# Performance work log

Measured on AMD Instinct MI355X. Metric: run time of the kernel, lower is better.

The kernel has to match this reference:

```python
import jax, jax.numpy as jnp
import numpy as np

N_NODES = 100000
N_EDGES = 3200000
N_FEAT = 128
DIM = 48
N_CLASS = 18
BN_EPS = 1e-5


def setup_inputs() -> dict:
    key = jax.random.key(0)
    ks = jax.random.split(key, 20)
    x = jax.random.normal(ks[0], (N_NODES, N_FEAT), dtype=jnp.float32)
    edge_index = jax.random.randint(ks[1], (2, N_EDGES), 0, N_NODES, dtype=jnp.int64)

    def lin(k, fan_in, fan_out):
        s = 1.0 / np.sqrt(fan_in)
        kw, kb = jax.random.split(k)
        W = jax.random.uniform(kw, (fan_in, fan_out), jnp.float32, -s, s)
        b = jax.random.uniform(kb, (fan_out,), jnp.float32, -s, s)
        return W, b

    c1_W1, c1_b1 = lin(ks[2], N_FEAT, DIM)
    c1_W2, c1_b2 = lin(ks[3], DIM, DIM)
    c2_W1, c2_b1 = lin(ks[4], DIM, DIM)
    c2_W2, c2_b2 = lin(ks[5], DIM, DIM)
    fc1_W, fc1_b = lin(ks[6], DIM, DIM)
    fc2_W, fc2_b = lin(ks[7], DIM, N_CLASS)

    def bn(k):
        k1, k2, k3, k4 = jax.random.split(k, 4)
        gamma = 1.0 + 0.1 * jax.random.normal(k1, (DIM,), jnp.float32)
        beta = 0.1 * jax.random.normal(k2, (DIM,), jnp.float32)
        mean = 0.1 * jax.random.normal(k3, (DIM,), jnp.float32)
        var = jax.random.uniform(k4, (DIM,), jnp.float32, 0.5, 1.5)
        return gamma, beta, mean, var

    bn1_g, bn1_b, bn1_m, bn1_v = bn(ks[8])
    bn2_g, bn2_b, bn2_m, bn2_v = bn(ks[9])

    return {
        "x": x, "edge_index": edge_index,
        "c1_W1": c1_W1, "c1_b1": c1_b1, "c1_W2": c1_W2, "c1_b2": c1_b2,
        "c2_W1": c2_W1, "c2_b1": c2_b1, "c2_W2": c2_W2, "c2_b2": c2_b2,
        "bn1_g": bn1_g, "bn1_b": bn1_b, "bn1_m": bn1_m, "bn1_v": bn1_v,
        "bn2_g": bn2_g, "bn2_b": bn2_b, "bn2_m": bn2_m, "bn2_v": bn2_v,
        "fc1_W": fc1_W, "fc1_b": fc1_b, "fc2_W": fc2_W, "fc2_b": fc2_b,
    }


def _gine_conv(x, src, dst, W1, b1, W2, b2, eps=0.0):
    # PyG GINEConv (edge_attr absent): message = ReLU(x_j), sum-aggregate to dst,
    # then nn((1+eps)*x + aggr) where nn = Linear-ReLU-Linear.
    msg = jax.nn.relu(x[src])                                  # [E, F]
    aggr = jax.ops.segment_sum(msg, dst, num_segments=x.shape[0])  # [N, F]
    h = (1.0 + eps) * x + aggr
    return jax.nn.relu(h @ W1 + b1) @ W2 + b2


def _bn_eval(x, gamma, beta, mean, var):
    return (x - mean) * (gamma * jax.lax.rsqrt(var + BN_EPS)) + beta


def reference(x, edge_index,
              c1_W1, c1_b1, c1_W2, c1_b2,
              c2_W1, c2_b1, c2_W2, c2_b2,
              bn1_g, bn1_b, bn1_m, bn1_v,
              bn2_g, bn2_b, bn2_m, bn2_v,
              fc1_W, fc1_b, fc2_W, fc2_b):
    src, dst = edge_index[0], edge_index[1]
    h = jax.nn.relu(_gine_conv(x, src, dst, c1_W1, c1_b1, c1_W2, c1_b2))
    h = _bn_eval(h, bn1_g, bn1_b, bn1_m, bn1_v)
    h = jax.nn.relu(_gine_conv(h, src, dst, c2_W1, c2_b1, c2_W2, c2_b2))
    h = _bn_eval(h, bn2_g, bn2_b, bn2_m, bn2_v)
    h = jax.nn.relu(h @ fc1_W + fc1_b)
    # dropout is identity in eval mode
    return h @ fc2_W + fc2_b
```

## Files before the change

### kernel.cpp

```cpp
#include <hip/hip_runtime.h>
#include <hip/hip_fp16.h>

#define N_NODES 100000
#define N_EDGES 3200000
#define N_FEAT  128
#define DIM     48
#define N_CLASS 18
#define BN_EPS  1e-5f

#define PADW 136
#define PADC 72
#define MROW 64

#define BSH    7
#define BROWS  128
#define NBUCK  ((N_NODES + BROWS - 1) / BROWS)
#define BCAP   4608
#define EPB    4096
#define NBLK_E ((N_EDGES + EPB - 1) / EPB)

typedef __attribute__((ext_vector_type(8))) _Float16 f16x8;
typedef __attribute__((ext_vector_type(4))) float f32x4;



__global__ __launch_bounds__(256) void k_bin(const int* __restrict__ ei,
                                             int* __restrict__ bcursor,
                                             unsigned int* __restrict__ pairs) {
    __shared__ int h[NBUCK];
    __shared__ int pos[NBUCK];
    const int t = threadIdx.x;
    const int bs = blockIdx.x * EPB;
    const int ce = min(EPB, N_EDGES - bs);

    int sv[16], dv[16];
    #pragma unroll
    for (int i = 0; i < 16; i++) {
        int e = t + i * 256;
        if (e < ce) { sv[i] = ei[bs + e]; dv[i] = ei[N_EDGES + bs + e]; }
        else { sv[i] = 0; dv[i] = -1; }
    }
    for (int i = t; i < NBUCK; i += 256) h[i] = 0;
    __syncthreads();
    #pragma unroll
    for (int i = 0; i < 16; i++)
        if (dv[i] >= 0) atomicAdd(&h[dv[i] >> BSH], 1);
    __syncthreads();

    for (int b = t; b < NBUCK; b += 256) {
        int cnt = h[b];
        if (cnt > 0) {
            int g = atomicAdd(&bcursor[b], cnt);
            h[b] = b * BCAP + g;
        }
        pos[b] = 0;
    }
    __syncthreads();

    #pragma unroll
    for (int i = 0; i < 16; i++) {
        if (dv[i] >= 0) {
            int b = dv[i] >> BSH;
            int p = atomicAdd(&pos[b], 1);
            pairs[h[b] + p] = ((unsigned int)sv[i] << 7) | (unsigned int)(dv[i] & (BROWS - 1));
        }
    }
}


__global__ __launch_bounds__(256) void k_sort(const unsigned int* __restrict__ pairs,
                                              const int* __restrict__ bcursor,
                                              int* __restrict__ row_beg,
                                              int* __restrict__ row_end,
                                              int* __restrict__ sorted_src) {
    __shared__ int histw[4 * BROWS];
    __shared__ int woff[4 * BROWS];
    __shared__ int tot[BROWS];
    __shared__ int scn[BROWS];
    __shared__ int beg[BROWS];
    const int t = threadIdx.x;
    const int wid = t >> 6;
    const int b = blockIdx.x;
    const int nbase = b << BSH;
    const int start_w = b * BCAP;
    const int cnt = bcursor[b];

    for (int i = t; i < 4 * BROWS; i += 256) histw[i] = 0;
    __syncthreads();
    for (int e = start_w + t; e < start_w + cnt; e += 256)
        atomicAdd(&histw[wid * BROWS + (pairs[e] & (BROWS - 1))], 1);
    __syncthreads();

    if (t < BROWS) {
        int run = 0;
        #pragma unroll
        for (int w = 0; w < 4; w++) {
            woff[w * BROWS + t] = run;
            run += histw[w * BROWS + t];
        }
        tot[t] = run;
        scn[t] = run;
    }
    __syncthreads();
    for (int off = 1; off < BROWS; off <<= 1) {
        int v = 0;
        if (t < BROWS && t >= off) v = scn[t - off];
        __syncthreads();
        if (t < BROWS) scn[t] += v;
        __syncthreads();
    }
    if (t < BROWS) {
        int rb = start_w + scn[t] - tot[t];
        beg[t] = rb;
        int n = nbase + t;
        if (n < N_NODES) {
            row_beg[n] = rb;
            row_end[n] = rb + tot[t];
        }
    }
    __syncthreads();
    if (t < BROWS) {
        #pragma unroll
        for (int w = 0; w < 4; w++)
            histw[w * BROWS + t] = beg[t] + woff[w * BROWS + t];
    }
    __syncthreads();
    for (int e = start_w + t; e < start_w + cnt; e += 256) {
        unsigned int p = pairs[e];
        int node = p & (BROWS - 1);
        int idx = atomicAdd(&histw[wid * BROWS + node], 1);
        sorted_src[idx] = (int)(p >> 7);
    }
}


__global__ __launch_bounds__(256) void k_g1(const float* __restrict__ x,
                                            const float* __restrict__ W1,
                                            __half* __restrict__ t1,
                                            __half* __restrict__ t2) {
    __shared__ _Float16 sX[64 * PADW];
    __shared__ _Float16 sW[DIM * PADW];
    const int t = threadIdx.x;
    const int base = blockIdx.x * 64;
    const int wid = t >> 6, lane = t & 63;

    for (int idx = t; idx < DIM * (N_FEAT / 2); idx += 256) {
        int c = idx >> 6;
        int kk = (idx & 63) * 2;
        *(__half2*)&sW[c * PADW + kk] =
            __floats2half2_rn(W1[kk * DIM + c], W1[(kk + 1) * DIM + c]);
    }
    #pragma unroll
    for (int i = 0; i < 8; i++) {
        int idx = t + i * 256;
        int row = idx >> 5, kq = idx & 31;
        float4 v = make_float4(0.f, 0.f, 0.f, 0.f);
        if (base + row < N_NODES) v = ((const float4*)x)[(base + row) * 32 + kq];
        *(__half2*)&sX[row * PADW + kq * 4]     = __floats2half2_rn(v.x, v.y);
        *(__half2*)&sX[row * PADW + kq * 4 + 2] = __floats2half2_rn(v.z, v.w);
    }
    __syncthreads();

    const int r16 = wid * 16;
    const int lrow = lane & 15;
    const int lk = (lane >> 4) * 8;

    f32x4 acc1[3], acc2[3];
    #pragma unroll
    for (int c = 0; c < 3; c++) {
        acc1[c] = (f32x4){0.f, 0.f, 0.f, 0.f};
        acc2[c] = (f32x4){0.f, 0.f, 0.f, 0.f};
    }

    #pragma unroll
    for (int ks = 0; ks < 4; ks++) {
        f16x8 a = *(const f16x8*)&sX[(r16 + lrow) * PADW + ks * 32 + lk];
        f16x8 ra;
        #pragma unroll
        for (int j = 0; j < 8; j++)
            ra[j] = a[j] > (_Float16)0 ? a[j] : (_Float16)0;
        #pragma unroll
        for (int c = 0; c < 3; c++) {
            f16x8 b = *(const f16x8*)&sW[(c * 16 + lrow) * PADW + ks * 32 + lk];
            acc1[c] = __builtin_amdgcn_mfma_f32_16x16x32_f16(a,  b, acc1[c], 0, 0, 0);
            acc2[c] = __builtin_amdgcn_mfma_f32_16x16x32_f16(ra, b, acc2[c], 0, 0, 0);
        }
    }

    const int orow = r16 + (lane >> 4) * 4;
    const int ocol = lane & 15;
    #pragma unroll
    for (int q = 0; q < 4; q++) {
        int gr = base + orow + q;
        if (gr < N_NODES) {
            #pragma unroll
            for (int c = 0; c < 3; c++) {
                t1[gr * DIM + c * 16 + ocol] = __float2half(acc1[c][q]);
                t2[gr * MROW + c * 16 + ocol] = __float2half(acc2[c][q]);
            }
        }
    }
}


__device__ inline float2 h2tof2(unsigned int u) {
    __half2 h = *reinterpret_cast<__half2*>(&u);
    return __half22float2(h);
}

__global__ __launch_bounds__(256) void k_aggr(const uint2* tl8,
                                              const uint2* __restrict__ tmsg8,
                                              const int* __restrict__ row_beg,
                                              const int* __restrict__ row_end,
                                              const int* __restrict__ ssrc,
                                              const float* __restrict__ bias,
                                              uint2* out8) {
    const int t = threadIdx.x;
    const int wid = t >> 6, lane = t & 63;
    const int sub = lane / 12;
    const int fl  = lane - sub * 12;
    int n = blockIdx.x * 20 + wid * 5 + sub;
    const bool act = (sub < 5) && (n < N_NODES);
    int start = 0, end = 0;
    if (act) { start = row_beg[n]; end = row_end[n]; }

    float ax = 0.f, ay = 0.f, az = 0.f, aw = 0.f;
    int e = start;
    for (; e + 8 <= end; e += 8) {
        int s0 = ssrc[e], s1 = ssrc[e + 1], s2 = ssrc[e + 2], s3 = ssrc[e + 3];
        int s4 = ssrc[e + 4], s5 = ssrc[e + 5], s6 = ssrc[e + 6], s7 = ssrc[e + 7];
        uint2 v0 = tmsg8[s0 * 16 + fl];
        uint2 v1 = tmsg8[s1 * 16 + fl];
        uint2 v2 = tmsg8[s2 * 16 + fl];
        uint2 v3 = tmsg8[s3 * 16 + fl];
        uint2 v4 = tmsg8[s4 * 16 + fl];
        uint2 v5 = tmsg8[s5 * 16 + fl];
        uint2 v6 = tmsg8[s6 * 16 + fl];
        uint2 v7 = tmsg8[s7 * 16 + fl];
        float2 f;
        f = h2tof2(v0.x); ax += f.x; ay += f.y;  f = h2tof2(v0.y); az += f.x; aw += f.y;
        f = h2tof2(v1.x); ax += f.x; ay += f.y;  f = h2tof2(v1.y); az += f.x; aw += f.y;
        f = h2tof2(v2.x); ax += f.x; ay += f.y;  f = h2tof2(v2.y); az += f.x; aw += f.y;
        f = h2tof2(v3.x); ax += f.x; ay += f.y;  f = h2tof2(v3.y); az += f.x; aw += f.y;
        f = h2tof2(v4.x); ax += f.x; ay += f.y;  f = h2tof2(v4.y); az += f.x; aw += f.y;
        f = h2tof2(v5.x); ax += f.x; ay += f.y;  f = h2tof2(v5.y); az += f.x; aw += f.y;
        f = h2tof2(v6.x); ax += f.x; ay += f.y;  f = h2tof2(v6.y); az += f.x; aw += f.y;
        f = h2tof2(v7.x); ax += f.x; ay += f.y;  f = h2tof2(v7.y); az += f.x; aw += f.y;
    }
    for (; e < end; e++) {
        int s = ssrc[e];
        uint2 v = tmsg8[s * 16 + fl];
        float2 f;
        f = h2tof2(v.x); ax += f.x; ay += f.y;
        f = h2tof2(v.y); az += f.x; aw += f.y;
    }
    if (act) {
        uint2 tv = tl8[n * 12 + fl];
        float2 b0 = h2tof2(tv.x), b1 = h2tof2(tv.y);
        float4 bi = ((const float4*)bias)[fl];
        float rx = fmaxf(b0.x + ax + bi.x, 0.f);
        float ry = fmaxf(b0.y + ay + bi.y, 0.f);
        float rz = fmaxf(b1.x + az + bi.z, 0.f);
        float rw = fmaxf(b1.y + aw + bi.w, 0.f);
        uint2 o;
        __half2 h0 = __floats2half2_rn(rx, ry);
        __half2 h1 = __floats2half2_rn(rz, rw);
        o.x = *reinterpret_cast<unsigned int*>(&h0);
        o.y = *reinterpret_cast<unsigned int*>(&h1);
        out8[n * 12 + fl] = o;
    }
}


__global__ __launch_bounds__(256) void k_chain1(const __half* u,
                                                const float* __restrict__ W2,
                                                const float* __restrict__ b2,
                                                const float* __restrict__ bng,
                                                const float* __restrict__ bnb,
                                                const float* __restrict__ bnm,
                                                const float* __restrict__ bnv,
                                                const float* __restrict__ W1n,
                                                __half* t3,
                                                __half* __restrict__ t4) {
    __shared__ _Float16 sU[64 * PADC];
    __shared__ _Float16 sG[64 * PADC];
    __shared__ _Float16 sW2t[DIM * PADC];
    __shared__ _Float16 sW1t[DIM * PADC];
    __shared__ float sb2[DIM], ssc[DIM], ssh[DIM];
    const int t = threadIdx.x;
    const int base = blockIdx.x * 64;
    const int wid = t >> 6, lane = t & 63;

    if (t < DIM) {
        sb2[t] = b2[t];
        float sc = bng[t] * rsqrtf(bnv[t] + BN_EPS);
        ssc[t] = sc;
        ssh[t] = bnb[t] - bnm[t] * sc;
    }
    for (int idx = t; idx < DIM * 24; idx += 256) {
        int c = idx / 24, kk = (idx - c * 24) * 2;
        sW2t[c * PADC + kk]     = (_Float16)W2[kk * DIM + c];
        sW2t[c * PADC + kk + 1] = (_Float16)W2[(kk + 1) * DIM + c];
        sW1t[c * PADC + kk]     = (_Float16)W1n[kk * DIM + c];
        sW1t[c * PADC + kk + 1] = (_Float16)W1n[(kk + 1) * DIM + c];
    }
    for (int idx = t; idx < DIM * 16; idx += 256) {
        int c = idx >> 4, j = idx & 15;
        sW2t[c * PADC + 48 + j] = (_Float16)0;
        sW1t[c * PADC + 48 + j] = (_Float16)0;
    }
    for (int idx = t; idx < 64 * 16; idx += 256) {
        int r = idx >> 4, j = idx & 15;
        sU[r * PADC + 48 + j] = (_Float16)0;
        sG[r * PADC + 48 + j] = (_Float16)0;
    }
    for (int idx = t; idx < 64 * 12; idx += 256) {
        int row = idx / 12, kk = idx - row * 12;
        uint2 v = make_uint2(0u, 0u);
        if (base + row < N_NODES) v = ((const uint2*)u)[(base + row) * 12 + kk];
        *(uint2*)&sU[row * PADC + kk * 4] = v;
    }
    __syncthreads();

    const int r16 = wid * 16;
    const int lrow = lane & 15;
    const int lk = (lane >> 4) * 8;
    const int orow = r16 + (lane >> 4) * 4;
    const int ocol = lane & 15;

    f32x4 av[3];
    #pragma unroll
    for (int c = 0; c < 3; c++) av[c] = (f32x4){0.f, 0.f, 0.f, 0.f};
    #pragma unroll
    for (int ks = 0; ks < 2; ks++) {
        f16x8 a = *(const f16x8*)&sU[(r16 + lrow) * PADC + ks * 32 + lk];
        #pragma unroll
        for (int c = 0; c < 3; c++) {
            f16x8 b = *(const f16x8*)&sW2t[(c * 16 + lrow) * PADC + ks * 32 + lk];
            av[c] = __builtin_amdgcn_mfma_f32_16x16x32_f16(a, b, av[c], 0, 0, 0);
        }
    }
    #pragma unroll
    for (int c = 0; c < 3; c++) {
        int col = c * 16 + ocol;
        float bb = sb2[col], sc = ssc[col], sh = ssh[col];
        #pragma unroll
        for (int q = 0; q < 4; q++) {
            float rl = fmaxf(av[c][q] + bb, 0.f);
            sG[(orow + q) * PADC + col] = (_Float16)(rl * sc + sh);
        }
    }
    __syncthreads();

    f32x4 a3[3], a4[3];
    #pragma unroll
    for (int c = 0; c < 3; c++) {
        a3[c] = (f32x4){0.f, 0.f, 0.f, 0.f};
        a4[c] = (f32x4){0.f, 0.f, 0.f, 0.f};
    }
    #pragma unroll
    for (int ks = 0; ks < 2; ks++) {
        f16x8 a = *(const f16x8*)&sG[(r16 + lrow) * PADC + ks * 32 + lk];
        f16x8 ra;
        #pragma unroll
        for (int j = 0; j < 8; j++)
            ra[j] = a[j] > (_Float16)0 ? a[j] : (_Float16)0;
        #pragma unroll
        for (int c = 0; c < 3; c++) {
            f16x8 b = *(const f16x8*)&sW1t[(c * 16 + lrow) * PADC + ks * 32 + lk];
            a3[c] = __builtin_amdgcn_mfma_f32_16x16x32_f16(a,  b, a3[c], 0, 0, 0);
            a4[c] = __builtin_amdgcn_mfma_f32_16x16x32_f16(ra, b, a4[c], 0, 0, 0);
        }
    }
    #pragma unroll
    for (int q = 0; q < 4; q++) {
        int gr = base + orow + q;
        if (gr < N_NODES) {
            #pragma unroll
            for (int c = 0; c < 3; c++) {
                t3[gr * DIM + c * 16 + ocol] = __float2half(a3[c][q]);
                t4[gr * MROW + c * 16 + ocol] = __float2half(a4[c][q]);
            }
        }
    }
}


__global__ __launch_bounds__(256) void k_chain2(const __half* __restrict__ u2,
                                                const float* __restrict__ W2,
                                                const float* __restrict__ b2,
                                                const float* __restrict__ bng,
                                                const float* __restrict__ bnb,
                                                const float* __restrict__ bnm,
                                                const float* __restrict__ bnv,
                                                const float* __restrict__ fc1W,
                                                const float* __restrict__ fc1b,
                                                const float* __restrict__ fc2W,
                                                const float* __restrict__ fc2b,
                                                float* __restrict__ out) {
    __shared__ _Float16 sA[64 * PADC];
    __shared__ _Float16 sG[64 * PADC];
    __shared__ _Float16 sWa[DIM * PADC];
    __shared__ _Float16 sWb[DIM * PADC];
    __shared__ _Float16 sWc[32 * PADC];
    __shared__ float sb2[DIM], ssc[DIM], ssh[DIM], sfb1[DIM], sfb2[N_CLASS];
    const int t = threadIdx.x;
    const int base = blockIdx.x * 64;
    const int wid = t >> 6, lane = t & 63;

    if (t < DIM) {
        sb2[t] = b2[t];
        float sc = bng[t] * rsqrtf(bnv[t] + BN_EPS);
        ssc[t] = sc;
        ssh[t] = bnb[t] - bnm[t] * sc;
        sfb1[t] = fc1b[t];
    }
    if (t >= 64 && t < 64 + N_CLASS) sfb2[t - 64] = fc2b[t - 64];

    for (int idx = t; idx < DIM * 24; idx += 256) {
        int c = idx / 24, kk = (idx - c * 24) * 2;
        sWa[c * PADC + kk]     = (_Float16)W2[kk * DIM + c];
        sWa[c * PADC + kk + 1] = (_Float16)W2[(kk + 1) * DIM + c];
        sWb[c * PADC + kk]     = (_Float16)fc1W[kk * DIM + c];
        sWb[c * PADC + kk + 1] = (_Float16)fc1W[(kk + 1) * DIM + c];
    }
    for (int idx = t; idx < DIM * 16; idx += 256) {
        int c = idx >> 4, j = idx & 15;
        sWa[c * PADC + 48 + j] = (_Float16)0;
        sWb[c * PADC + 48 + j] = (_Float16)0;
    }
    for (int idx = t; idx < N_CLASS * DIM; idx += 256) {
        int c = idx / DIM, k = idx - c * DIM;
        sWc[c * PADC + k] = (_Float16)fc2W[k * N_CLASS + c];
    }
    for (int idx = t; idx < 32 * 16; idx += 256) {
        int c = idx >> 4, j = idx & 15;
        sWc[c * PADC + 48 + j] = (_Float16)0;
    }
    for (int idx = t; idx < 14 * 48; idx += 256) {
        int c = 18 + idx / 48, k = idx - (idx / 48) * 48;
        sWc[c * PADC + k] = (_Float16)0;
    }
    for (int idx = t; idx < 64 * 16; idx += 256) {
        int r = idx >> 4, j = idx & 15;
        sA[r * PADC + 48 + j] = (_Float16)0;
        sG[r * PADC + 48 + j] = (_Float16)0;
    }
    for (int idx = t; idx < 64 * 12; idx += 256) {
        int row = idx / 12, kk = idx - row * 12;
        uint2 v = make_uint2(0u, 0u);
        if (base + row < N_NODES) v = ((const uint2*)u2)[(base + row) * 12 + kk];
        *(uint2*)&sA[row * PADC + kk * 4] = v;
    }
    __syncthreads();

    const int r16 = wid * 16;
    const int lrow = lane & 15;
    const int lk = (lane >> 4) * 8;
    const int orow = r16 + (lane >> 4) * 4;
    const int ocol = lane & 15;

    {
        f32x4 av[3];
        #pragma unroll
        for (int c = 0; c < 3; c++) av[c] = (f32x4){0.f, 0.f, 0.f, 0.f};
        #pragma unroll
        for (int ks = 0; ks < 2; ks++) {
            f16x8 a = *(const f16x8*)&sA[(r16 + lrow) * PADC + ks * 32 + lk];
            #pragma unroll
            for (int c = 0; c < 3; c++) {
                f16x8 b = *(const f16x8*)&sWa[(c * 16 + lrow) * PADC + ks * 32 + lk];
                av[c] = __builtin_amdgcn_mfma_f32_16x16x32_f16(a, b, av[c], 0, 0, 0);
            }
        }
        #pragma unroll
        for (int c = 0; c < 3; c++) {
            int col = c * 16 + ocol;
            float bb = sb2[col], sc = ssc[col], sh = ssh[col];
            #pragma unroll
            for (int q = 0; q < 4; q++) {
                float rl = fmaxf(av[c][q] + bb, 0.f);
                sG[(orow + q) * PADC + col] = (_Float16)(rl * sc + sh);
            }
        }
    }
    __syncthreads();

    {
        f32x4 az[3];
        #pragma unroll
        for (int c = 0; c < 3; c++) az[c] = (f32x4){0.f, 0.f, 0.f, 0.f};
        #pragma unroll
        for (int ks = 0; ks < 2; ks++) {
            f16x8 a = *(const f16x8*)&sG[(r16 + lrow) * PADC + ks * 32 + lk];
            #pragma unroll
            for (int c = 0; c < 3; c++) {
                f16x8 b = *(const f16x8*)&sWb[(c * 16 + lrow) * PADC + ks * 32 + lk];
                az[c] = __builtin_amdgcn_mfma_f32_16x16x32_f16(a, b, az[c], 0, 0, 0);
            }
        }
        __syncthreads();
        #pragma unroll
        for (int c = 0; c < 3; c++) {
            int col = c * 16 + ocol;
            float bb = sfb1[col];
            #pragma unroll
            for (int q = 0; q < 4; q++)
                sA[(orow + q) * PADC + col] = (_Float16)fmaxf(az[c][q] + bb, 0.f);
        }
    }
    __syncthreads();

    {
        f32x4 ao[2];
        #pragma unroll
        for (int c = 0; c < 2; c++) ao[c] = (f32x4){0.f, 0.f, 0.f, 0.f};
        #pragma unroll
        for (int ks = 0; ks < 2; ks++) {
            f16x8 a = *(const f16x8*)&sA[(r16 + lrow) * PADC + ks * 32 + lk];
            #pragma unroll
            for (int c = 0; c < 2; c++) {
                f16x8 b = *(const f16x8*)&sWc[(c * 16 + lrow) * PADC + ks * 32 + lk];
                ao[c] = __builtin_amdgcn_mfma_f32_16x16x32_f16(a, b, ao[c], 0, 0, 0);
            }
        }
        #pragma unroll
        for (int q = 0; q < 4; q++) {
            int gr = base + orow + q;
            if (gr < N_NODES) {
                #pragma unroll
                for (int c = 0; c < 2; c++) {
                    int col = c * 16 + ocol;
                    if (col < N_CLASS)
                        out[gr * N_CLASS + col] = ao[c][q] + sfb2[col];
                }
            }
        }
    }
}


extern "C" void kernel_launch(void* const* d_in, const int* in_sizes, int n_in,
                              void* d_out, int out_size, void* d_ws, size_t ws_size,
                              hipStream_t stream) {
    const float* x     = (const float*)d_in[0];
    const int*   ei    = (const int*)d_in[1];
    const float* c1_W1 = (const float*)d_in[2];
    const float* c1_b1 = (const float*)d_in[3];
    const float* c1_W2 = (const float*)d_in[4];
    const float* c1_b2 = (const float*)d_in[5];
    const float* c2_W1 = (const float*)d_in[6];
    const float* c2_b1 = (const float*)d_in[7];
    const float* c2_W2 = (const float*)d_in[8];
    const float* c2_b2 = (const float*)d_in[9];
    const float* bn1_g = (const float*)d_in[10];
    const float* bn1_b = (const float*)d_in[11];
    const float* bn1_m = (const float*)d_in[12];
    const float* bn1_v = (const float*)d_in[13];
    const float* bn2_g = (const float*)d_in[14];
    const float* bn2_b = (const float*)d_in[15];
    const float* bn2_m = (const float*)d_in[16];
    const float* bn2_v = (const float*)d_in[17];
    const float* fc1_W = (const float*)d_in[18];
    const float* fc1_b = (const float*)d_in[19];
    const float* fc2_W = (const float*)d_in[20];
    const float* fc2_b = (const float*)d_in[21];
    float* out = (float*)d_out;

    char* ws = (char*)d_ws;
    size_t o = 0;
    auto take = [&](size_t bytes) {
        void* p = ws + o;
        o = (o + bytes + 255) & ~(size_t)255;
        return p;
    };
    unsigned int* pairs = (unsigned int*)take((size_t)NBUCK * BCAP * 4);
    int*  sorted_src    = (int*)take((size_t)NBUCK * BCAP * 4);
    int*  row_beg       = (int*)take((size_t)N_NODES * 4);
    int*  row_end       = (int*)take((size_t)N_NODES * 4);
    int*  bcursor       = (int*)take((size_t)NBUCK * 4);
    __half* t1h         = (__half*)take((size_t)N_NODES * DIM * 2);
    __half* t2h         = (__half*)take((size_t)N_NODES * MROW * 2);
    (void)ws_size; (void)in_sizes; (void)n_in; (void)out_size;

    const int NB64 = (N_NODES + 63) / 64;
    const int NB20 = (N_NODES + 19) / 20;

    hipMemsetAsync(bcursor, 0, (size_t)NBUCK * 4, stream);
    k_bin<<<NBLK_E, 256, 0, stream>>>(ei, bcursor, pairs);
    k_sort<<<NBUCK, 256, 0, stream>>>(pairs, bcursor, row_beg, row_end, sorted_src);

    k_g1<<<NB64, 256, 0, stream>>>(x, c1_W1, t1h, t2h);
    k_aggr<<<NB20, 256, 0, stream>>>((const uint2*)t1h, (const uint2*)t2h,
                                     row_beg, row_end, sorted_src, c1_b1, (uint2*)t1h);
    k_chain1<<<NB64, 256, 0, stream>>>(t1h, c1_W2, c1_b2, bn1_g, bn1_b, bn1_m, bn1_v,
                                       c2_W1, t1h, t2h);
    k_aggr<<<NB20, 256, 0, stream>>>((const uint2*)t1h, (const uint2*)t2h,
                                     row_beg, row_end, sorted_src, c2_b1, (uint2*)t1h);
    k_chain2<<<NB64, 256, 0, stream>>>(t1h, c2_W2, c2_b2, bn2_g, bn2_b, bn2_m, bn2_v,
                                       fc1_W, fc1_b, fc2_W, fc2_b, out);
}
```

Before: 265.8 us.

## Merge bucket sort and first GEMM into one launch; halve edges per bin block

The per-bucket sort kernel and the first dense transform kernel become one launch. Block indices below NBUCK run the sort and the rest run the GEMM, with a shared-memory buffer reused between the two roles. Because the two pieces of work are independent, this removes one launch and lets them overlap on the GPU. Edges per block in the binning kernel are also halved, which doubles the block count and reduces per-thread registers, at the cost of more global bucket-cursor atomics.

```diff
diff --git a/kernel.cpp b/kernel.cpp
--- a/kernel.cpp
+++ b/kernel.cpp
@@ -16,8 +16,10 @@
 #define BROWS  128
 #define NBUCK  ((N_NODES + BROWS - 1) / BROWS)
 #define BCAP   4608
-#define EPB    4096
+#define EPB    2048
 #define NBLK_E ((N_EDGES + EPB - 1) / EPB)
+
+#define NB64   ((N_NODES + 63) / 64)
 
 typedef __attribute__((ext_vector_type(8))) _Float16 f16x8;
 typedef __attribute__((ext_vector_type(4))) float f32x4;
@@ -33,9 +35,9 @@
     const int bs = blockIdx.x * EPB;
     const int ce = min(EPB, N_EDGES - bs);
 
-    int sv[16], dv[16];
-    #pragma unroll
-    for (int i = 0; i < 16; i++) {
+    int sv[8], dv[8];
+    #pragma unroll
+    for (int i = 0; i < 8; i++) {
         int e = t + i * 256;
         if (e < ce) { sv[i] = ei[bs + e]; dv[i] = ei[N_EDGES + bs + e]; }
         else { sv[i] = 0; dv[i] = -1; }
@@ -43,7 +45,7 @@
     for (int i = t; i < NBUCK; i += 256) h[i] = 0;
     __syncthreads();
     #pragma unroll
-    for (int i = 0; i < 16; i++)
+    for (int i = 0; i < 8; i++)
         if (dv[i] >= 0) atomicAdd(&h[dv[i] >> BSH], 1);
     __syncthreads();
 
@@ -58,7 +60,7 @@
     __syncthreads();
 
     #pragma unroll
-    for (int i = 0; i < 16; i++) {
+    for (int i = 0; i < 8; i++) {
         if (dv[i] >= 0) {
             int b = dv[i] >> BSH;
             int p = atomicAdd(&pos[b], 1);
@@ -68,135 +70,136 @@
 }
 
 
-__global__ __launch_bounds__(256) void k_sort(const unsigned int* __restrict__ pairs,
-                                              const int* __restrict__ bcursor,
-                                              int* __restrict__ row_beg,
-                                              int* __restrict__ row_end,
-                                              int* __restrict__ sorted_src) {
-    __shared__ int histw[4 * BROWS];
-    __shared__ int woff[4 * BROWS];
-    __shared__ int tot[BROWS];
-    __shared__ int scn[BROWS];
-    __shared__ int beg[BROWS];
+__global__ __launch_bounds__(256) void k_sortg1(const unsigned int* __restrict__ pairs,
+                                                const int* __restrict__ bcursor,
+                                                int* __restrict__ row_beg,
+                                                int* __restrict__ row_end,
+                                                int* __restrict__ sorted_src,
+                                                const float* __restrict__ x,
+                                                const float* __restrict__ W1,
+                                                __half* __restrict__ t1,
+                                                __half* __restrict__ t2) {
+    __shared__ __align__(16) char smem[30720];
     const int t = threadIdx.x;
-    const int wid = t >> 6;
-    const int b = blockIdx.x;
-    const int nbase = b << BSH;
-    const int start_w = b * BCAP;
-    const int cnt = bcursor[b];
-
-    for (int i = t; i < 4 * BROWS; i += 256) histw[i] = 0;
-    __syncthreads();
-    for (int e = start_w + t; e < start_w + cnt; e += 256)
-        atomicAdd(&histw[wid * BROWS + (pairs[e] & (BROWS - 1))], 1);
-    __syncthreads();
-
-    if (t < BROWS) {
-        int run = 0;
-        #pragma unroll
-        for (int w = 0; w < 4; w++) {
-            woff[w * BROWS + t] = run;
-            run += histw[w * BROWS + t];
-        }
-        tot[t] = run;
-        scn[t] = run;
-    }
-    __syncthreads();
-    for (int off = 1; off < BROWS; off <<= 1) {
-        int v = 0;
-        if (t < BROWS && t >= off) v = scn[t - off];
+
+    if (blockIdx.x < NBUCK) {
+        int* histw = (int*)smem;
+        int* woff  = (int*)(smem + 2048);
+        int* tot   = (int*)(smem + 4096);
+        int* scn   = (int*)(smem + 4608);
+        int* beg   = (int*)(smem + 5120);
+        const int wid = t >> 6;
+        const int b = blockIdx.x;
+        const int nbase = b << BSH;
+        const int start_w = b * BCAP;
+        const int cnt = bcursor[b];
+
+        for (int i = t; i < 4 * BROWS; i += 256) histw[i] = 0;
         __syncthreads();
-        if (t < BROWS) scn[t] += v;
+        for (int e = start_w + t; e < start_w + cnt; e += 256)
+            atomicAdd(&histw[wid * BROWS + (pairs[e] & (BROWS - 1))], 1);
         __syncthreads();
-    }
-    if (t < BROWS) {
-        int rb = start_w + scn[t] - tot[t];
-        beg[t] = rb;
-        int n = nbase + t;
-        if (n < N_NODES) {
-            row_beg[n] = rb;
-            row_end[n] = rb + tot[t];
-        }
-    }
-    __syncthreads();
-    if (t < BROWS) {
-        #pragma unroll
-        for (int w = 0; w < 4; w++)
-            histw[w * BROWS + t] = beg[t] + woff[w * BROWS + t];
-    }
-    __syncthreads();
-    for (int e = start_w + t; e < start_w + cnt; e += 256) {
-        unsigned int p = pairs[e];
-        int node = p & (BROWS - 1);
-        int idx = atomicAdd(&histw[wid * BROWS + node], 1);
-        sorted_src[idx] = (int)(p >> 7);
-    }
-}
-
-
-__global__ __launch_bounds__(256) void k_g1(const float* __restrict__ x,
-                                            const float* __restrict__ W1,
-                                            __half* __restrict__ t1,
-                                            __half* __restrict__ t2) {
-    __shared__ _Float16 sX[64 * PADW];
-    __shared__ _Float16 sW[DIM * PADW];
-    const int t = threadIdx.x;
-    const int base = blockIdx.x * 64;
-    const int wid = t >> 6, lane = t & 63;
-
-    for (int idx = t; idx < DIM * (N_FEAT / 2); idx += 256) {
-        int c = idx >> 6;
-        int kk = (idx & 63) * 2;
-        *(__half2*)&sW[c * PADW + kk] =
-            __floats2half2_rn(W1[kk * DIM + c], W1[(kk + 1) * DIM + c]);
-    }
-    #pragma unroll
-    for (int i = 0; i < 8; i++) {
-        int idx = t + i * 256;
-        int row = idx >> 5, kq = idx & 31;
-        float4 v = make_float4(0.f, 0.f, 0.f, 0.f);
-        if (base + row < N_NODES) v = ((const float4*)x)[(base + row) * 32 + kq];
-        *(__half2*)&sX[row * PADW + kq * 4]     = __floats2half2_rn(v.x, v.y);
-        *(__half2*)&sX[row * PADW + kq * 4 + 2] = __floats2half2_rn(v.z, v.w);
-    }
-    __syncthreads();
-
-    const int r16 = wid * 16;
-    const int lrow = lane & 15;
-    const int lk = (lane >> 4) * 8;
-
-    f32x4 acc1[3], acc2[3];
-    #pragma unroll
-    for (int c = 0; c < 3; c++) {
-        acc1[c] = (f32x4){0.f, 0.f, 0.f, 0.f};
-        acc2[c] = (f32x4){0.f, 0.f, 0.f, 0.f};
-    }
-
-    #pragma unroll
-    for (int ks = 0; ks < 4; ks++) {
-        f16x8 a = *(const f16x8*)&sX[(r16 + lrow) * PADW + ks * 32 + lk];
-        f16x8 ra;
-        #pragma unroll
-        for (int j = 0; j < 8; j++)
-            ra[j] = a[j] > (_Float16)0 ? a[j] : (_Float16)0;
+
+        if (t < BROWS) {
+            int run = 0;
+            #pragma unroll
+            for (int w = 0; w < 4; w++) {
+                woff[w * BROWS + t] = run;
+                run += histw[w * BROWS + t];
+            }
+            tot[t] = run;
+            scn[t] = run;
+        }
+        __syncthreads();
+        for (int off = 1; off < BROWS; off <<= 1) {
+            int v = 0;
+            if (t < BROWS && t >= off) v = scn[t - off];
+            __syncthreads();
+            if (t < BROWS) scn[t] += v;
+            __syncthreads();
+        }
+        if (t < BROWS) {
+            int rb = start_w + scn[t] - tot[t];
+            beg[t] = rb;
+            int n = nbase + t;
+            if (n < N_NODES) {
+                row_beg[n] = rb;
+                row_end[n] = rb + tot[t];
+            }
+        }
+        __syncthreads();
+        if (t < BROWS) {
+            #pragma unroll
+            for (int w = 0; w < 4; w++)
+                histw[w * BROWS + t] = beg[t] + woff[w * BROWS + t];
+        }
+        __syncthreads();
+        for (int e = start_w + t; e < start_w + cnt; e += 256) {
+            unsigned int p = pairs[e];
+            int node = p & (BROWS - 1);
+            int idx = atomicAdd(&histw[wid * BROWS + node], 1);
+            sorted_src[idx] = (int)(p >> 7);
+        }
+    } else {
+        _Float16* sX = (_Float16*)smem;
+        _Float16* sW = (_Float16*)(smem + 64 * PADW * 2);
+        const int base = (blockIdx.x - NBUCK) * 64;
+        const int wid = t >> 6, lane = t & 63;
+
+        for (int idx = t; idx < DIM * (N_FEAT / 2); idx += 256) {
+            int c = idx >> 6;
+            int kk = (idx & 63) * 2;
+            *(__half2*)&sW[c * PADW + kk] =
+                __floats2half2_rn(W1[kk * DIM + c], W1[(kk + 1) * DIM + c]);
+        }
+        #pragma unroll
+        for (int i = 0; i < 8; i++) {
+            int idx = t + i * 256;
+            int row = idx >> 5, kq = idx & 31;
+            float4 v = make_float4(0.f, 0.f, 0.f, 0.f);
+            if (base + row < N_NODES) v = ((const float4*)x)[(base + row) * 32 + kq];
+            *(__half2*)&sX[row * PADW + kq * 4]     = __floats2half2_rn(v.x, v.y);
+            *(__half2*)&sX[row * PADW + kq * 4 + 2] = __floats2half2_rn(v.z, v.w);
+        }
+        __syncthreads();
+
+        const int r16 = wid * 16;
+        const int lrow = lane & 15;
+        const int lk = (lane >> 4) * 8;
+
+        f32x4 acc1[3], acc2[3];
         #pragma unroll
         for (int c = 0; c < 3; c++) {
-            f16x8 b = *(const f16x8*)&sW[(c * 16 + lrow) * PADW + ks * 32 + lk];
-            acc1[c] = __builtin_amdgcn_mfma_f32_16x16x32_f16(a,  b, acc1[c], 0, 0, 0);
-            acc2[c] = __builtin_amdgcn_mfma_f32_16x16x32_f16(ra, b, acc2[c], 0, 0, 0);
-        }
-    }
-
-    const int orow = r16 + (lane >> 4) * 4;
-    const int ocol = lane & 15;
-    #pragma unroll
-    for (int q = 0; q < 4; q++) {
-        int gr = base + orow + q;
-        if (gr < N_NODES) {
+            acc1[c] = (f32x4){0.f, 0.f, 0.f, 0.f};
+            acc2[c] = (f32x4){0.f, 0.f, 0.f, 0.f};
+        }
+
+        #pragma unroll
+        for (int ks = 0; ks < 4; ks++) {
+            f16x8 a = *(const f16x8*)&sX[(r16 + lrow) * PADW + ks * 32 + lk];
+            f16x8 ra;
+            #pragma unroll
+            for (int j = 0; j < 8; j++)
+                ra[j] = a[j] > (_Float16)0 ? a[j] : (_Float16)0;
             #pragma unroll
             for (int c = 0; c < 3; c++) {
-                t1[gr * DIM + c * 16 + ocol] = __float2half(acc1[c][q]);
-                t2[gr * MROW + c * 16 + ocol] = __float2half(acc2[c][q]);
+                f16x8 b = *(const f16x8*)&sW[(c * 16 + lrow) * PADW + ks * 32 + lk];
+                acc1[c] = __builtin_amdgcn_mfma_f32_16x16x32_f16(a,  b, acc1[c], 0, 0, 0);
+                acc2[c] = __builtin_amdgcn_mfma_f32_16x16x32_f16(ra, b, acc2[c], 0, 0, 0);
+            }
+        }
+
+        const int orow = r16 + (lane >> 4) * 4;
+        const int ocol = lane & 15;
+        #pragma unroll
+        for (int q = 0; q < 4; q++) {
+            int gr = base + orow + q;
+            if (gr < N_NODES) {
+                #pragma unroll
+                for (int c = 0; c < 3; c++) {
+                    t1[gr * DIM + c * 16 + ocol] = __float2half(acc1[c][q]);
+                    t2[gr * MROW + c * 16 + ocol] = __float2half(acc2[c][q]);
+                }
             }
         }
     }
@@ -583,14 +586,12 @@
     __half* t2h         = (__half*)take((size_t)N_NODES * MROW * 2);
     (void)ws_size; (void)in_sizes; (void)n_in; (void)out_size;
 
-    const int NB64 = (N_NODES + 63) / 64;
     const int NB20 = (N_NODES + 19) / 20;
 
     hipMemsetAsync(bcursor, 0, (size_t)NBUCK * 4, stream);
     k_bin<<<NBLK_E, 256, 0, stream>>>(ei, bcursor, pairs);
-    k_sort<<<NBUCK, 256, 0, stream>>>(pairs, bcursor, row_beg, row_end, sorted_src);
-
-    k_g1<<<NB64, 256, 0, stream>>>(x, c1_W1, t1h, t2h);
+    k_sortg1<<<NBUCK + NB64, 256, 0, stream>>>(pairs, bcursor, row_beg, row_end, sorted_src,
+                                               x, c1_W1, t1h, t2h);
     k_aggr<<<NB20, 256, 0, stream>>>((const uint2*)t1h, (const uint2*)t2h,
                                      row_beg, row_end, sorted_src, c1_b1, (uint2*)t1h);
     k_chain1<<<NB64, 256, 0, stream>>>(t1h, c1_W2, c1_b2, bn1_g, bn1_b, bn1_m, bn1_v,
```

New measurement: 272.7 us. 1.03x slower.
